# Optimization experiments

Measured on AMD Instinct MI355X. Metric: run time of the kernel, lower is better.

The kernel has to match this reference:

```python
import jax, jax.numpy as jnp
import numpy as np

T, D, L, H = 512, 256, 256, 512  # tokens, embed dim, lstm dims, hidden units


def _lstm(x, W, U, b):
    """Keras-style LSTM over x [T, Din] -> hidden states [T, L].
    Gate order i, f, g(cell), o; sigmoid recurrent activations, tanh cell."""
    Ldim = U.shape[0]

    def step(carry, xt):
        h, c = carry
        z = xt @ W + h @ U + b  # [4L]
        i, f, g, o = jnp.split(z, 4)
        i = jax.nn.sigmoid(i)
        f = jax.nn.sigmoid(f)
        g = jnp.tanh(g)
        o = jax.nn.sigmoid(o)
        c = f * c + i * g
        h = o * jnp.tanh(c)
        return (h, c), h

    h0 = jnp.zeros((Ldim,), x.dtype)
    _, hs = jax.lax.scan(step, (h0, h0), x)
    return hs


def setup_inputs() -> dict:
    key = jax.random.key(0)
    ks = jax.random.split(key, 16)

    def p(k, shape):
        # Glorot-like small init
        fan = shape[0] + shape[-1]
        return jax.random.normal(k, shape, jnp.float32) * np.float32(np.sqrt(2.0 / fan))

    return {
        "embeddings": jax.random.normal(ks[0], (1, T, D), jnp.float32),
        "W_f1": p(ks[1], (D, 4 * L)), "U_f1": p(ks[2], (L, 4 * L)), "b_f1": jnp.zeros((4 * L,), jnp.float32),
        "W_b1": p(ks[3], (D, 4 * L)), "U_b1": p(ks[4], (L, 4 * L)), "b_b1": jnp.zeros((4 * L,), jnp.float32),
        "W_f2": p(ks[5], (2 * L, 4 * L)), "U_f2": p(ks[6], (L, 4 * L)), "b_f2": jnp.zeros((4 * L,), jnp.float32),
        "W_b2": p(ks[7], (2 * L, 4 * L)), "U_b2": p(ks[8], (L, 4 * L)), "b_b2": jnp.zeros((4 * L,), jnp.float32),
        "FOH": p(ks[9], (2 * L, H)),
        "FOM": p(ks[10], (2 * L, H)),
        "hidBias": p(ks[11], (1, H)),
        "outLayer": p(ks[12], (H, 1)),
        "outBias": p(ks[13], (1, 1)),
    }


def reference(embeddings, W_f1, U_f1, b_f1, W_b1, U_b1, b_b1,
              W_f2, U_f2, b_f2, W_b2, U_b2, b_b2,
              FOH, FOM, hidBias, outLayer, outBias):
    x = embeddings[0]  # [T, D]
    # --- FirstBiLSTMModule ---
    rf1 = _lstm(x, W_f1, U_f1, b_f1)            # forward LSTM over sequence
    rb1 = _lstm(x[::-1], W_b1, U_b1, b_b1)      # backward LSTM over reversed sequence
    # concatenate_layers: pair forward step i with backward step T-1-i
    v = jnp.concatenate([rf1, rb1[::-1]], axis=-1)  # [T, 2L]
    # --- NextBiLSTMModule ---
    rf2 = _lstm(v, W_f2, U_f2, b_f2)
    rb2 = _lstm(v[::-1], W_b2, U_b2, b_b2)
    hcat = jnp.concatenate([rf2, rb2[::-1]], axis=-1)  # [T, 2L] per-token concat
    # --- ConcatHeadModule.__evaluate (hidden2_units == 0 path) ---
    headfov = hcat @ FOH  # [T, H]
    modfov = hcat @ FOM   # [T, H]
    # pairwise: activation(headfov_i + modfov_j + hidBias) @ outLayer + outBias
    act = jnp.tanh(headfov[:, None, :] + modfov[None, :, :] + hidBias[0])  # [T, T, H]
    scores = jnp.einsum('ijh,ho->ij', act, outLayer) + outBias[0, 0]       # [T, T]
    return scores
```

## Files before the change

kernel.cpp:

```cpp
#include <hip/hip_runtime.h>
#include <hip/hip_bf16.h>


typedef _Float16 h2v __attribute__((ext_vector_type(2)));
typedef unsigned int u32x8 __attribute__((ext_vector_type(8)));

#define BC(x) __builtin_bit_cast(h2v, (x))

__device__ __forceinline__ float fdot2f(h2v a, h2v b, float c) {
#if __has_builtin(__builtin_amdgcn_fdot2)
    return __builtin_amdgcn_fdot2(a, b, c, false);
#else
    return c + (float)a[0] * (float)b[0] + (float)a[1] * (float)b[1];
#endif
}

__global__ __launch_bounds__(256) void prep_u(const float* __restrict__ U,
                                              unsigned int* __restrict__ Uf) {
    int idx = blockIdx.x * 256 + threadIdx.x;
    int k2 = idx >> 10, col = idx & 1023;
    union { _Float16 h[2]; unsigned int u; } p;
    p.h[0] = (_Float16)U[(2 * k2) * 1024 + col];
    p.h[1] = (_Float16)U[(2 * k2 + 1) * 1024 + col];
    Uf[idx] = p.u;
}

__global__ __launch_bounds__(256) void gemm_bias(const float* __restrict__ A,
                                                 const float* __restrict__ B,
                                                 const float* __restrict__ bias,
                                                 float* __restrict__ C,
                                                 int M, int N, int K, int revA) {
    __shared__ float sA[16][65];
    __shared__ float sB[16][65];
    int tid = threadIdx.x;
    int bm = blockIdx.y * 64, bn = blockIdx.x * 64;
    int tx = tid & 15, ty = tid >> 4;
    float acc[4][4] = {};
    for (int k0 = 0; k0 < K; k0 += 16) {
#pragma unroll
        for (int l = 0; l < 4; l++) {
            int flat = tid + 256 * l;
            int ml = flat >> 4, kk = flat & 15;
            int row = bm + ml;
            if (revA) row = M - 1 - row;
            sA[kk][ml] = A[row * K + k0 + kk];
        }
#pragma unroll
        for (int l = 0; l < 4; l++) {
            int flat = tid + 256 * l;
            int kk = flat >> 6, nl = flat & 63;
            sB[kk][nl] = B[(k0 + kk) * N + bn + nl];
        }
        __syncthreads();
#pragma unroll
        for (int kk = 0; kk < 16; kk++) {
            float a[4], b[4];
#pragma unroll
            for (int i = 0; i < 4; i++) a[i] = sA[kk][ty + 16 * i];
#pragma unroll
            for (int j = 0; j < 4; j++) b[j] = sB[kk][tx + 16 * j];
#pragma unroll
            for (int i = 0; i < 4; i++)
#pragma unroll
                for (int j = 0; j < 4; j++) acc[i][j] += a[i] * b[j];
        }
        __syncthreads();
    }
#pragma unroll
    for (int i = 0; i < 4; i++) {
        int r = bm + ty + 16 * i;
#pragma unroll
        for (int j = 0; j < 4; j++) {
            int cidx = bn + tx + 16 * j;
            float bv = bias ? bias[cidx] : 0.f;
            C[r * N + cidx] = acc[i][j] + bv;
        }
    }
}

#define KLDS 32
#define KREG 96

#define UA(r) ((r) < 8 ? qa0[(r) & 7] : (r) < 16 ? qa1[(r) & 7] : (r) < 24 ? qa2[(r) & 7] : \
               (r) < 32 ? qa3[(r) & 7] : (r) < 40 ? qa4[(r) & 7] : (r) < 48 ? qa5[(r) & 7] : \
               (r) < 56 ? qa6[(r) & 7] : (r) < 64 ? qa7[(r) & 7] : (r) < 72 ? qa8[(r) & 7] : \
               (r) < 80 ? qa9[(r) & 7] : (r) < 88 ? qa10[(r) & 7] : qa11[(r) & 7])
#define UB(r) ((r) < 8 ? qb0[(r) & 7] : (r) < 16 ? qb1[(r) & 7] : (r) < 24 ? qb2[(r) & 7] : \
               (r) < 32 ? qb3[(r) & 7] : (r) < 40 ? qb4[(r) & 7] : (r) < 48 ? qb5[(r) & 7] : \
               (r) < 56 ? qb6[(r) & 7] : (r) < 64 ? qb7[(r) & 7] : (r) < 72 ? qb8[(r) & 7] : \
               (r) < 80 ? qb9[(r) & 7] : (r) < 88 ? qb10[(r) & 7] : qb11[(r) & 7])

#define LOADQ(q, va, vb)                                                      \
    do {                                                                      \
        _Pragma("unroll") for (int j = 0; j < 8; j++) {                       \
            uint2 w = *(const uint2*)&U[(KLDS + 8 * (q) + j) * 1024 + 2 * t]; \
            va[j] = w.x;                                                      \
            vb[j] = w.y;                                                      \
        }                                                                     \
    } while (0)

__global__ __attribute__((amdgpu_flat_work_group_size(512, 512),
                          amdgpu_waves_per_eu(2, 2)))
void lstm_two(
        const unsigned int* __restrict__ Ua, const unsigned int* __restrict__ Ub,
        const float* __restrict__ Pa, const float* __restrict__ Pb,
        float* __restrict__ Oa, float* __restrict__ Ob) {
    const unsigned int* U = blockIdx.x ? Ub : Ua;
    const float* P = blockIdx.x ? Pb : Pa;
    float* O = blockIdx.x ? Ob : Oa;

    __shared__ unsigned int sU[KLDS * 1024];
    __shared__ __align__(16) _Float16 sH[256];
    __shared__ float sZ[1024];

    int t = threadIdx.x;

    for (int i = t; i < KLDS * 1024; i += 512) sU[i] = U[i];

    u32x8 qa0, qa1, qa2, qa3, qa4, qa5, qa6, qa7, qa8, qa9, qa10, qa11;
    u32x8 qb0, qb1, qb2, qb3, qb4, qb5, qb6, qb7, qb8, qb9, qb10, qb11;
    LOADQ(0, qa0, qb0);   LOADQ(1, qa1, qb1);   LOADQ(2, qa2, qb2);
    LOADQ(3, qa3, qb3);   LOADQ(4, qa4, qb4);   LOADQ(5, qa5, qb5);
    LOADQ(6, qa6, qb6);   LOADQ(7, qa7, qb7);   LOADQ(8, qa8, qb8);
    LOADQ(9, qa9, qb9);   LOADQ(10, qa10, qb10); LOADQ(11, qa11, qb11);

    asm volatile(""
                 : "+v"(qa0), "+v"(qa1), "+v"(qa2), "+v"(qa3), "+v"(qa4),
                   "+v"(qa5), "+v"(qa6), "+v"(qa7), "+v"(qa8), "+v"(qa9),
                   "+v"(qa10), "+v"(qa11), "+v"(qb0), "+v"(qb1), "+v"(qb2),
                   "+v"(qb3), "+v"(qb4), "+v"(qb5), "+v"(qb6), "+v"(qb7),
                   "+v"(qb8), "+v"(qb9), "+v"(qb10), "+v"(qb11));

    float c = 0.f;
    if (t < 256) sH[t] = (_Float16)0.f;
    __syncthreads();

    const uint4* hp4 = (const uint4*)sH;
    float2 pc = *(const float2*)(P + 2 * t);
    for (int step = 0; step < 512; step++) {
        float2 pn = pc;
        if (step < 511) pn = *(const float2*)(P + (step + 1) * 1024 + 2 * t);
        float acc0 = pc.x, acc1 = pc.y;

#pragma unroll
        for (int cch = 0; cch < 8; cch++) {
            uint4 hc = hp4[cch];
            const unsigned int* su = &sU[(4 * cch) * 1024 + 2 * t];
            uint2 w;
            w = *(const uint2*)(su);
            acc0 = fdot2f(BC(hc.x), BC(w.x), acc0);
            acc1 = fdot2f(BC(hc.x), BC(w.y), acc1);
            w = *(const uint2*)(su + 1024);
            acc0 = fdot2f(BC(hc.y), BC(w.x), acc0);
            acc1 = fdot2f(BC(hc.y), BC(w.y), acc1);
            w = *(const uint2*)(su + 2048);
            acc0 = fdot2f(BC(hc.z), BC(w.x), acc0);
            acc1 = fdot2f(BC(hc.z), BC(w.y), acc1);
            w = *(const uint2*)(su + 3072);
            acc0 = fdot2f(BC(hc.w), BC(w.x), acc0);
            acc1 = fdot2f(BC(hc.w), BC(w.y), acc1);
        }
#pragma unroll
        for (int cch = 0; cch < 24; cch++) {
            uint4 hc = hp4[8 + cch];
            const int r0 = 4 * cch;
            acc0 = fdot2f(BC(hc.x), BC(UA(r0 + 0)), acc0);
            acc1 = fdot2f(BC(hc.x), BC(UB(r0 + 0)), acc1);
            acc0 = fdot2f(BC(hc.y), BC(UA(r0 + 1)), acc0);
            acc1 = fdot2f(BC(hc.y), BC(UB(r0 + 1)), acc1);
            acc0 = fdot2f(BC(hc.z), BC(UA(r0 + 2)), acc0);
            acc1 = fdot2f(BC(hc.z), BC(UB(r0 + 2)), acc1);
            acc0 = fdot2f(BC(hc.w), BC(UA(r0 + 3)), acc0);
            acc1 = fdot2f(BC(hc.w), BC(UB(r0 + 3)), acc1);
        }
        ((float2*)sZ)[t] = make_float2(acc0, acc1);
        __syncthreads();
        if (t < 256) {
            float zi = sZ[t], zf = sZ[256 + t], zg = sZ[512 + t], zo = sZ[768 + t];
            float ig = 1.f / (1.f + __expf(-zi));
            float fg = 1.f / (1.f + __expf(-zf));
            float gg = 1.f - 2.f / (1.f + __expf(2.f * zg));
            float og = 1.f / (1.f + __expf(-zo));
            c = fg * c + ig * gg;
            float h = og * (1.f - 2.f / (1.f + __expf(2.f * c)));
            O[step * 256 + t] = h;
            sH[t] = (_Float16)h;
        }
        __syncthreads();
        pc = pn;
    }
}

__global__ __launch_bounds__(256) void concat_k(const float* __restrict__ F,
                                                const float* __restrict__ Bk,
                                                float* __restrict__ V) {
    int idx = blockIdx.x * 256 + threadIdx.x;
    int t = idx >> 9, d = idx & 511;
    V[idx] = (d < 256) ? F[t * 256 + d] : Bk[(511 - t) * 256 + d - 256];
}

__global__ __launch_bounds__(256) void head_kernel(const float* __restrict__ HF,
                                                   const float* __restrict__ MF,
                                                   const float* __restrict__ w,
                                                   const float* __restrict__ outb,
                                                   float* __restrict__ S) {
    int i = blockIdx.x;
    __shared__ float sHF[512], sW[512];
    int tid = threadIdx.x;
    sHF[tid] = HF[i * 512 + tid];
    sHF[tid + 256] = HF[i * 512 + 256 + tid];
    sW[tid] = w[tid];
    sW[tid + 256] = w[tid + 256];
    __syncthreads();
    int lane = tid & 63, wv = tid >> 6;
    float ob = outb[0];
    for (int j = wv; j < 512; j += 4) {
        const float* mf = MF + j * 512;
        float acc = 0.f;
#pragma unroll
        for (int r = 0; r < 8; r++) {
            int h = lane + 64 * r;
            float x = sHF[h] + mf[h];
            acc += sW[h] * (1.f - 2.f / (1.f + __expf(2.f * x)));
        }
#pragma unroll
        for (int off = 32; off; off >>= 1) acc += __shfl_down(acc, off);
        if (lane == 0) S[i * 512 + j] = acc + ob;
    }
}

extern "C" void kernel_launch(void* const* d_in, const int* in_sizes, int n_in,
                              void* d_out, int out_size, void* d_ws, size_t ws_size,
                              hipStream_t stream) {
    const float* emb      = (const float*)d_in[0];
    const float* W_f1     = (const float*)d_in[1];
    const float* U_f1     = (const float*)d_in[2];
    const float* b_f1     = (const float*)d_in[3];
    const float* W_b1     = (const float*)d_in[4];
    const float* U_b1     = (const float*)d_in[5];
    const float* b_b1     = (const float*)d_in[6];
    const float* W_f2     = (const float*)d_in[7];
    const float* U_f2     = (const float*)d_in[8];
    const float* b_f2     = (const float*)d_in[9];
    const float* W_b2     = (const float*)d_in[10];
    const float* U_b2     = (const float*)d_in[11];
    const float* b_b2     = (const float*)d_in[12];
    const float* FOH      = (const float*)d_in[13];
    const float* FOM      = (const float*)d_in[14];
    const float* hidBias  = (const float*)d_in[15];
    const float* outLayer = (const float*)d_in[16];
    const float* outBias  = (const float*)d_in[17];
    float* out = (float*)d_out;

    unsigned int* uf = (unsigned int*)d_ws;
    unsigned int* uf_f1 = uf;
    unsigned int* uf_b1 = uf + 131072;
    unsigned int* uf_f2 = uf + 262144;
    unsigned int* uf_b2 = uf + 393216;
    float* f = (float*)d_ws + 524288;
    float* P1f = f;
    float* P1b = f + 524288;
    float* P2f = f + 1048576;
    float* P2b = f + 1572864;
    float* rf1 = f + 2097152;
    float* rb1 = f + 2228224;
    float* rf2 = f + 2359296;
    float* rb2 = f + 2490368;
    float* v    = f + 2621440;
    float* hcat = f + 2883584;
    float* HFb  = f + 3145728;
    float* MFb  = f + 3407872;

    prep_u<<<512, 256, 0, stream>>>(U_f1, uf_f1);
    prep_u<<<512, 256, 0, stream>>>(U_b1, uf_b1);
    prep_u<<<512, 256, 0, stream>>>(U_f2, uf_f2);
    prep_u<<<512, 256, 0, stream>>>(U_b2, uf_b2);

    dim3 g1(1024 / 64, 512 / 64);
    gemm_bias<<<g1, 256, 0, stream>>>(emb, W_f1, b_f1, P1f, 512, 1024, 256, 0);
    gemm_bias<<<g1, 256, 0, stream>>>(emb, W_b1, b_b1, P1b, 512, 1024, 256, 1);

    lstm_two<<<2, 512, 0, stream>>>(uf_f1, uf_b1, P1f, P1b, rf1, rb1);

    concat_k<<<1024, 256, 0, stream>>>(rf1, rb1, v);

    gemm_bias<<<g1, 256, 0, stream>>>(v, W_f2, b_f2, P2f, 512, 1024, 512, 0);
    gemm_bias<<<g1, 256, 0, stream>>>(v, W_b2, b_b2, P2b, 512, 1024, 512, 1);

    lstm_two<<<2, 512, 0, stream>>>(uf_f2, uf_b2, P2f, P2b, rf2, rb2);

    concat_k<<<1024, 256, 0, stream>>>(rf2, rb2, hcat);

    dim3 g2(512 / 64, 512 / 64);
    gemm_bias<<<g2, 256, 0, stream>>>(hcat, FOH, hidBias, HFb, 512, 512, 512, 0);
    gemm_bias<<<g2, 256, 0, stream>>>(hcat, FOM, nullptr, MFb, 512, 512, 512, 0);

    head_kernel<<<512, 256, 0, stream>>>(HFb, MFb, outLayer, outBias, out);
}
```

Baseline: 2.756 ms.

## Split recurrent weights across LDS, registers and per-step global/L2 loads

Repartitions the fp16-packed recurrent matrix U across three tiers. LDS grows from 32 to 36 packed rows, registers shrink from 96 to 40 rows, and the last 52 rows are reloaded from global memory (expected to hit cache) on every timestep. The aim is to cut VGPR pressure, and possible spilling, from holding 192 registers of weights per thread. The cost is global/L2 latency on the serial recurrence path each step, plus more LDS use.

After: 2.822 ms. 2.4% more time.

```diff
diff --git a/kernel.cpp b/kernel.cpp
--- a/kernel.cpp
+++ b/kernel.cpp
@@ -78,22 +78,18 @@
     }
 }
 
-#define KLDS 32
-#define KREG 96
+#define KLDS 36
+#define KREG 40
 
 #define UA(r) ((r) < 8 ? qa0[(r) & 7] : (r) < 16 ? qa1[(r) & 7] : (r) < 24 ? qa2[(r) & 7] : \
-               (r) < 32 ? qa3[(r) & 7] : (r) < 40 ? qa4[(r) & 7] : (r) < 48 ? qa5[(r) & 7] : \
-               (r) < 56 ? qa6[(r) & 7] : (r) < 64 ? qa7[(r) & 7] : (r) < 72 ? qa8[(r) & 7] : \
-               (r) < 80 ? qa9[(r) & 7] : (r) < 88 ? qa10[(r) & 7] : qa11[(r) & 7])
+               (r) < 32 ? qa3[(r) & 7] : qa4[(r) & 7])
 #define UB(r) ((r) < 8 ? qb0[(r) & 7] : (r) < 16 ? qb1[(r) & 7] : (r) < 24 ? qb2[(r) & 7] : \
-               (r) < 32 ? qb3[(r) & 7] : (r) < 40 ? qb4[(r) & 7] : (r) < 48 ? qb5[(r) & 7] : \
-               (r) < 56 ? qb6[(r) & 7] : (r) < 64 ? qb7[(r) & 7] : (r) < 72 ? qb8[(r) & 7] : \
-               (r) < 80 ? qb9[(r) & 7] : (r) < 88 ? qb10[(r) & 7] : qb11[(r) & 7])
-
-#define LOADQ(q, va, vb)                                                      \
+               (r) < 32 ? qb3[(r) & 7] : qb4[(r) & 7])
+
+#define LOADQ(qi, va, vb)                                                     \
     do {                                                                      \
         _Pragma("unroll") for (int j = 0; j < 8; j++) {                       \
-            uint2 w = *(const uint2*)&U[(KLDS + 8 * (q) + j) * 1024 + 2 * t]; \
+            uint2 w = *(const uint2*)&U[(KLDS + 8 * (qi) + j) * 1024 + 2 * t]; \
             va[j] = w.x;                                                      \
             vb[j] = w.y;                                                      \
         }                                                                     \
@@ -117,19 +113,17 @@
 
     for (int i = t; i < KLDS * 1024; i += 512) sU[i] = U[i];
 
-    u32x8 qa0, qa1, qa2, qa3, qa4, qa5, qa6, qa7, qa8, qa9, qa10, qa11;
-    u32x8 qb0, qb1, qb2, qb3, qb4, qb5, qb6, qb7, qb8, qb9, qb10, qb11;
-    LOADQ(0, qa0, qb0);   LOADQ(1, qa1, qb1);   LOADQ(2, qa2, qb2);
-    LOADQ(3, qa3, qb3);   LOADQ(4, qa4, qb4);   LOADQ(5, qa5, qb5);
-    LOADQ(6, qa6, qb6);   LOADQ(7, qa7, qb7);   LOADQ(8, qa8, qb8);
-    LOADQ(9, qa9, qb9);   LOADQ(10, qa10, qb10); LOADQ(11, qa11, qb11);
+    u32x8 qa0, qa1, qa2, qa3, qa4;
+    u32x8 qb0, qb1, qb2, qb3, qb4;
+    LOADQ(0, qa0, qb0);
+    LOADQ(1, qa1, qb1);
+    LOADQ(2, qa2, qb2);
+    LOADQ(3, qa3, qb3);
+    LOADQ(4, qa4, qb4);
 
     asm volatile(""
                  : "+v"(qa0), "+v"(qa1), "+v"(qa2), "+v"(qa3), "+v"(qa4),
-                   "+v"(qa5), "+v"(qa6), "+v"(qa7), "+v"(qa8), "+v"(qa9),
-                   "+v"(qa10), "+v"(qa11), "+v"(qb0), "+v"(qb1), "+v"(qb2),
-                   "+v"(qb3), "+v"(qb4), "+v"(qb5), "+v"(qb6), "+v"(qb7),
-                   "+v"(qb8), "+v"(qb9), "+v"(qb10), "+v"(qb11));
+                   "+v"(qb0), "+v"(qb1), "+v"(qb2), "+v"(qb3), "+v"(qb4));
 
     float c = 0.f;
     if (t < 256) sH[t] = (_Float16)0.f;
@@ -143,7 +137,7 @@
         float acc0 = pc.x, acc1 = pc.y;
 
 #pragma unroll
-        for (int cch = 0; cch < 8; cch++) {
+        for (int cch = 0; cch < 9; cch++) {
             uint4 hc = hp4[cch];
             const unsigned int* su = &sU[(4 * cch) * 1024 + 2 * t];
             uint2 w;
@@ -161,9 +155,9 @@
             acc1 = fdot2f(BC(hc.w), BC(w.y), acc1);
         }
 #pragma unroll
-        for (int cch = 0; cch < 24; cch++) {
-            uint4 hc = hp4[8 + cch];
-            const int r0 = 4 * cch;
+        for (int cch = 9; cch < 19; cch++) {
+            uint4 hc = hp4[cch];
+            const int r0 = 4 * (cch - 9);
             acc0 = fdot2f(BC(hc.x), BC(UA(r0 + 0)), acc0);
             acc1 = fdot2f(BC(hc.x), BC(UB(r0 + 0)), acc1);
             acc0 = fdot2f(BC(hc.y), BC(UA(r0 + 1)), acc0);
@@ -172,6 +166,23 @@
             acc1 = fdot2f(BC(hc.z), BC(UB(r0 + 2)), acc1);
             acc0 = fdot2f(BC(hc.w), BC(UA(r0 + 3)), acc0);
             acc1 = fdot2f(BC(hc.w), BC(UB(r0 + 3)), acc1);
+        }
+#pragma unroll
+        for (int cch = 19; cch < 32; cch++) {
+            uint4 hc = hp4[cch];
+            const unsigned int* ug = &U[(4 * cch) * 1024 + 2 * t];
+            uint2 w0 = *(const uint2*)(ug);
+            uint2 w1 = *(const uint2*)(ug + 1024);
+            uint2 w2 = *(const uint2*)(ug + 2048);
+            uint2 w3 = *(const uint2*)(ug + 3072);
+            acc0 = fdot2f(BC(hc.x), BC(w0.x), acc0);
+            acc1 = fdot2f(BC(hc.x), BC(w0.y), acc1);
+            acc0 = fdot2f(BC(hc.y), BC(w1.x), acc0);
+            acc1 = fdot2f(BC(hc.y), BC(w1.y), acc1);
+            acc0 = fdot2f(BC(hc.z), BC(w2.x), acc0);
+            acc1 = fdot2f(BC(hc.z), BC(w2.y), acc1);
+            acc0 = fdot2f(BC(hc.w), BC(w3.x), acc0);
+            acc1 = fdot2f(BC(hc.w), BC(w3.y), acc1);
         }
         ((float2*)sZ)[t] = make_float2(acc0, acc1);
         __syncthreads();
```
